# Optimization experiments

Hardware: AMD Instinct MI355X
Metric: run time of the kernel (lower is better)

The kernel has to match this reference:

```python
import jax, jax.numpy as jnp
import numpy as np

B, C, H, W_IMG, P, D = 64, 3, 224, 224, 16, 768
N_PATCH = (H // P) * (W_IMG // P)  # 196
SEQ = N_PATCH + 1                  # 197


def setup_inputs() -> dict:
    key = jax.random.key(0)
    k1, k2, k3, k4, k5 = jax.random.split(key, 5)
    in_feat = P * P * C  # 768
    return {
        "x": jax.random.normal(k1, (B, C, H, W_IMG), dtype=jnp.float32),
        "W": jax.random.normal(k2, (in_feat, D), dtype=jnp.float32) * (1.0 / np.sqrt(in_feat)),
        "b": jax.random.normal(k3, (D,), dtype=jnp.float32) * 0.02,
        "pos_table": jax.random.normal(k4, (SEQ, D), dtype=jnp.float32) * 0.02,
        "class_token": jax.random.normal(k5, (1, 1, D), dtype=jnp.float32),
    }


def _patchify(x):
    # Matches torch loop: patch (i,j) is x[:, :, i*P:(i+1)*P, j*P:(j+1)*P].reshape(B, C*P*P)
    # i.e. features ordered channel-major then row then col within patch.
    b = x.shape[0]
    hp, wp = H // P, W_IMG // P
    x = x.reshape(b, C, hp, P, wp, P)              # (B,C,hp,P,wp,P)
    x = x.transpose(0, 2, 4, 1, 3, 5)              # (B,hp,wp,C,P,P)
    return x.reshape(b, hp * wp, C * P * P)        # (B,N,C*P*P)


def reference(x, W, b, pos_table, class_token):
    patches = _patchify(x)                          # (B, N, C*P*P)
    tokens = jnp.einsum("bnf,fd->bnd", patches, W) + b  # (B, N, D)
    cls = jnp.broadcast_to(class_token, (x.shape[0], 1, D))
    seq = jnp.concatenate([cls, tokens], axis=1)    # (B, SEQ, D)
    # positions = arange(SEQ) broadcast over batch -> embedding lookup
    return seq + pos_table[None, :, :]              # dropout is identity in eval
```

## Files before the change

kernel.cpp:

```cpp
#include <hip/hip_runtime.h>
#include <hip/hip_bf16.h>

namespace {

constexpr int Bsz = 64, Cch = 3, Himg = 224, Wimg = 224, Ppat = 16;
constexpr int Dm = 768, NPW = 14, NPATCH = 196, SEQn = 197;
constexpr int Mtot = Bsz * NPATCH;
constexpr int Ktot = 768, Ntot = 768;
constexpr int BM = 64, BN = 128, BK = 64;
constexpr int MT = Mtot / BM;
constexpr int NT = Ntot / BN;
constexpr int KT = Ktot / BK;
constexpr int NBLK = MT * NT;
constexpr int TA = BM * BK;
constexpr int TB = BN * BK;
constexpr size_t AP_ELEMS = (size_t)MT * KT * TA;
constexpr size_t WT_ELEMS = (size_t)NT * KT * TB;
constexpr size_t WS_NEED = (AP_ELEMS + WT_ELEMS) * 2;
constexpr int WPREP_BLK = (Ktot / 8) * Ntot / 256;
constexpr int CLS_BLK = Bsz * Dm / 256;

typedef __attribute__((ext_vector_type(8))) short bf16x8;
typedef __attribute__((ext_vector_type(4))) float f32x4;

__device__ inline unsigned short f2bf(float f) {
  __bf16 h = (__bf16)f;
  union { __bf16 h; unsigned short u; } c;
  c.h = h;
  return c.u;
}

__global__ void prep_kernel(const float* __restrict__ x, const float* __restrict__ W,
                            const float* __restrict__ pos, const float* __restrict__ cls,
                            unsigned short* __restrict__ Ap, unsigned short* __restrict__ Wt,
                            float* __restrict__ out, int nPatchBlk) {
  __shared__ unsigned short tile[TA];
  const int bid = blockIdx.x;
  const int t = threadIdx.x;
  if (bid < nPatchBlk) {
    int mt = bid / KT, kt = bid - mt * KT;
    int ml = t >> 2, ks = t & 3;
    int m = mt * BM + ml;
    int b = m / NPATCH;
    int pidx = m - b * NPATCH;
    int ph = pidx / NPW, pw = pidx - ph * NPW;
    int kbase = kt * BK + ks * 16;
    int c = kbase >> 8, pi = (kbase >> 4) & 15;
    const float* src = x + (((size_t)(b * Cch + c) * Himg + ph * Ppat + pi) * Wimg + pw * Ppat);
#pragma unroll
    for (int j = 0; j < 4; ++j) {
      float4 v = *reinterpret_cast<const float4*>(src + 4 * j);
      int idx = (ml * BK + ks * 16 + 4 * j) ^ ((ml & 7) << 3);
      *reinterpret_cast<ushort4*>(&tile[idx]) =
          make_ushort4(f2bf(v.x), f2bf(v.y), f2bf(v.z), f2bf(v.w));
    }
    __syncthreads();
    const uint4* sp = reinterpret_cast<const uint4*>(tile);
    uint4* dp = reinterpret_cast<uint4*>(Ap + (size_t)bid * TA);
    dp[t] = sp[t];
    dp[t + 256] = sp[t + 256];
  } else if (bid < nPatchBlk + WPREP_BLK) {
    int cid = (bid - nPatchBlk) * 256 + t;
    int kc = cid / Ntot;
    int n = cid - kc * Ntot;
    int nb = n >> 7;
    int np = n & 127;
    int kt = kc >> 3;
    int k8 = (kc & 7) * 8;
    unsigned short tmp[8];
#pragma unroll
    for (int j = 0; j < 8; ++j) tmp[j] = f2bf(W[(kc * 8 + j) * Ntot + n]);
    int idx = np * BK + k8;
    int sidx = idx ^ ((np & 7) << 3);
    unsigned short* dst = Wt + (size_t)(nb * KT + kt) * TB + sidx;
    *reinterpret_cast<ushort4*>(dst + 0) = make_ushort4(tmp[0], tmp[1], tmp[2], tmp[3]);
    *reinterpret_cast<ushort4*>(dst + 4) = make_ushort4(tmp[4], tmp[5], tmp[6], tmp[7]);
  } else {
    int i = (bid - nPatchBlk - WPREP_BLK) * 256 + t;
    int b = i / Dm;
    int d = i - b * Dm;
    out[(size_t)b * (SEQn * Dm) + d] = cls[d] + pos[d];
  }
}

__global__ __launch_bounds__(256, 3)
void gemm_kernel(const unsigned short* __restrict__ Ap, const unsigned short* __restrict__ Wt,
                 const float* __restrict__ bias, const float* __restrict__ pos,
                 float* __restrict__ out) {
  __shared__ unsigned short A[2][TA];
  __shared__ unsigned short B[2][TB];

  const int orig = blockIdx.x;
  const int wg = (orig & 7) * (NBLK / 8) + (orig >> 3);
  const int bm = wg / NT;
  const int bn = wg - bm * NT;

  const int t = threadIdx.x;
  const int lane = t & 63;
  const int wid = t >> 6;
  const int wr = wid >> 1, wc = wid & 1;
  const int fr = lane & 15, fq = lane >> 4;

  const unsigned short* aSrc = Ap + (size_t)(bm * KT) * TA + t * 8;
  const unsigned short* bSrc = Wt + (size_t)(bn * KT) * TB + t * 8;

  auto STAGEA = [&](int buf, int kt) {
#pragma unroll
    for (int i = 0; i < 2; ++i)
      __builtin_amdgcn_global_load_lds(
          (const __attribute__((address_space(1))) unsigned int*)(aSrc + kt * TA + i * 2048),
          (__attribute__((address_space(3))) unsigned int*)(&A[buf][t * 8 + i * 2048]),
          16, 0, 0);
  };
  auto STAGEB = [&](int buf, int kt) {
#pragma unroll
    for (int i = 0; i < 4; ++i)
      __builtin_amdgcn_global_load_lds(
          (const __attribute__((address_space(1))) unsigned int*)(bSrc + kt * TB + i * 2048),
          (__attribute__((address_space(3))) unsigned int*)(&B[buf][t * 8 + i * 2048]),
          16, 0, 0);
  };

  f32x4 acc[2][4];
#pragma unroll
  for (int mi = 0; mi < 2; ++mi)
#pragma unroll
    for (int ni = 0; ni < 4; ++ni) acc[mi][ni] = {0.f, 0.f, 0.f, 0.f};

  STAGEA(0, 0);
  STAGEB(0, 0);
  __syncthreads();

  for (int kt = 0; kt < KT; ++kt) {
    const int cur = kt & 1, nxt = cur ^ 1;
    if (kt + 1 < KT) {
      STAGEA(nxt, kt + 1);
      STAGEB(nxt, kt + 1);
    }
#pragma unroll
    for (int ks = 0; ks < 2; ++ks) {
      bf16x8 af[2], bfr[4];
#pragma unroll
      for (int mi = 0; mi < 2; ++mi) {
        int row = wr * 32 + mi * 16 + fr;
        int idx = (row * BK + ks * 32 + fq * 8) ^ ((row & 7) << 3);
        af[mi] = *reinterpret_cast<const bf16x8*>(&A[cur][idx]);
      }
#pragma unroll
      for (int ni = 0; ni < 4; ++ni) {
        int n = wc * 64 + ni * 16 + fr;
        int idx = (n * BK + ks * 32 + fq * 8) ^ ((n & 7) << 3);
        bfr[ni] = *reinterpret_cast<const bf16x8*>(&B[cur][idx]);
      }
#pragma unroll
      for (int mi = 0; mi < 2; ++mi)
#pragma unroll
        for (int ni = 0; ni < 4; ++ni)
          acc[mi][ni] = __builtin_amdgcn_mfma_f32_16x16x32_bf16(
              af[mi], bfr[ni], acc[mi][ni], 0, 0, 0);
    }
    __syncthreads();
  }

  const int n0 = bn * BN + wc * 64;
  float bv[4];
#pragma unroll
  for (int ni = 0; ni < 4; ++ni) bv[ni] = bias[n0 + ni * 16 + fr];
#pragma unroll
  for (int mi = 0; mi < 2; ++mi) {
#pragma unroll
    for (int j = 0; j < 4; ++j) {
      int m = bm * BM + wr * 32 + mi * 16 + fq * 4 + j;
      int b = m / NPATCH;
      int s = m - b * NPATCH + 1;
      float* orow = out + ((size_t)b * SEQn + s) * Dm + n0;
      const float* prow = pos + (size_t)s * Dm + n0;
#pragma unroll
      for (int ni = 0; ni < 4; ++ni) {
        int d = ni * 16 + fr;
        orow[d] = acc[mi][ni][j] + bv[ni] + prow[d];
      }
    }
  }
}

__global__ __launch_bounds__(512, 6)
void gemm_fb(const float* __restrict__ x, const unsigned short* __restrict__ Wt,
             const float* __restrict__ bias, const float* __restrict__ pos,
             float* __restrict__ out) {
  __shared__ unsigned short As[2][TA];
  __shared__ unsigned short Bs[2][TB];

  const int orig = blockIdx.x;
  const int wg = (orig & 7) * (NBLK / 8) + (orig >> 3);
  const int bm = wg / NT;
  const int bn = wg - bm * NT;

  const int t = threadIdx.x;
  const int lane = t & 63;
  const int wid = t >> 6;
  const int wr = wid >> 2, wc = wid & 3;
  const int fr = lane & 15, fq = lane >> 4;

  const int c4 = t & 15;
  const int r0 = t >> 4;
  int a_base[2];
#pragma unroll
  for (int i = 0; i < 2; ++i) {
    int m = bm * BM + r0 + 32 * i;
    int b = m / NPATCH;
    int pidx = m - b * NPATCH;
    int ph = pidx / NPW;
    int pw = pidx - ph * NPW;
    a_base[i] = ((b * Cch) * Himg + ph * Ppat) * Wimg + pw * Ppat;
  }
  const unsigned short* wt_base = Wt + (size_t)bn * (KT * TB);

  float4 av[2];
  auto LOADA = [&](int kt) {
    int kg = kt * BK + c4 * 4;
    int c = kg >> 8;
    int pi = (kg >> 4) & 15;
    int pj = kg & 15;
    int off = (c * Himg + pi) * Wimg + pj;
#pragma unroll
    for (int i = 0; i < 2; ++i)
      av[i] = *reinterpret_cast<const float4*>(x + a_base[i] + off);
  };
  auto WRITEA = [&](int buf) {
#pragma unroll
    for (int i = 0; i < 2; ++i) {
      int row = r0 + 32 * i;
      int idx = (row * BK + c4 * 4) ^ ((row & 7) << 3);
      ushort4 pk = make_ushort4(f2bf(av[i].x), f2bf(av[i].y), f2bf(av[i].z), f2bf(av[i].w));
      *reinterpret_cast<ushort4*>(&As[buf][idx]) = pk;
    }
  };
  auto STAGEB = [&](int buf, int kt) {
    const unsigned short* src = wt_base + kt * TB + t * 8;
#pragma unroll
    for (int i = 0; i < 2; ++i) {
      __builtin_amdgcn_global_load_lds(
          (const __attribute__((address_space(1))) unsigned int*)(src + i * 4096),
          (__attribute__((address_space(3))) unsigned int*)(&Bs[buf][t * 8 + i * 4096]),
          16, 0, 0);
    }
  };

  f32x4 acc[2][2];
#pragma unroll
  for (int mi = 0; mi < 2; ++mi)
#pragma unroll
    for (int ni = 0; ni < 2; ++ni) acc[mi][ni] = {0.f, 0.f, 0.f, 0.f};

  LOADA(0);
  STAGEB(0, 0);
  WRITEA(0);
  __syncthreads();

  for (int kt = 0; kt < KT; ++kt) {
    const int cur = kt & 1, nxt = cur ^ 1;
    if (kt + 1 < KT) {
      LOADA(kt + 1);
      STAGEB(nxt, kt + 1);
    }
#pragma unroll
    for (int ks = 0; ks < 2; ++ks) {
      bf16x8 af[2], bfr[2];
#pragma unroll
      for (int mi = 0; mi < 2; ++mi) {
        int row = wr * 32 + mi * 16 + fr;
        int idx = (row * BK + ks * 32 + fq * 8) ^ ((row & 7) << 3);
        af[mi] = *reinterpret_cast<const bf16x8*>(&As[cur][idx]);
      }
#pragma unroll
      for (int ni = 0; ni < 2; ++ni) {
        int n = wc * 32 + ni * 16 + fr;
        int idx = (n * BK + ks * 32 + fq * 8) ^ ((n & 7) << 3);
        bfr[ni] = *reinterpret_cast<const bf16x8*>(&Bs[cur][idx]);
      }
#pragma unroll
      for (int mi = 0; mi < 2; ++mi)
#pragma unroll
        for (int ni = 0; ni < 2; ++ni)
          acc[mi][ni] = __builtin_amdgcn_mfma_f32_16x16x32_bf16(
              af[mi], bfr[ni], acc[mi][ni], 0, 0, 0);
    }
    if (kt + 1 < KT) WRITEA(nxt);
    __syncthreads();
  }

  const int n0 = bn * BN + wc * 32;
  float bv[2];
#pragma unroll
  for (int ni = 0; ni < 2; ++ni) bv[ni] = bias[n0 + ni * 16 + fr];
#pragma unroll
  for (int mi = 0; mi < 2; ++mi) {
#pragma unroll
    for (int j = 0; j < 4; ++j) {
      int m = bm * BM + wr * 32 + mi * 16 + fq * 4 + j;
      int b = m / NPATCH;
      int s = m - b * NPATCH + 1;
      float* orow = out + ((size_t)b * SEQn + s) * Dm + n0;
      const float* prow = pos + (size_t)s * Dm + n0;
#pragma unroll
      for (int ni = 0; ni < 2; ++ni) {
        int d = ni * 16 + fr;
        orow[d] = acc[mi][ni][j] + bv[ni] + prow[d];
      }
    }
  }
}

}

extern "C" void kernel_launch(void* const* d_in, const int* in_sizes, int n_in,
                              void* d_out, int out_size, void* d_ws, size_t ws_size,
                              hipStream_t stream) {
  const float* x = (const float*)d_in[0];
  const float* W = (const float*)d_in[1];
  const float* bias = (const float*)d_in[2];
  const float* pos = (const float*)d_in[3];
  const float* cls = (const float*)d_in[4];
  float* out = (float*)d_out;

  const bool pure = ws_size >= WS_NEED;
  unsigned short* Ap = (unsigned short*)d_ws;
  unsigned short* Wt = pure ? Ap + AP_ELEMS : Ap;
  const int nPatchBlk = pure ? MT * KT : 0;

  prep_kernel<<<nPatchBlk + WPREP_BLK + CLS_BLK, 256, 0, stream>>>(
      x, W, pos, cls, Ap, Wt, out, nPatchBlk);
  if (pure)
    gemm_kernel<<<NBLK, 256, 0, stream>>>(Ap, Wt, bias, pos, out);
  else
    gemm_fb<<<NBLK, 512, 0, stream>>>(x, Wt, bias, pos, out);
}
```

Baseline: 44.79 us.

## Enlarge GEMM M-tile to 128 and write patch tiles directly without LDS

Doubles the GEMM block tile in M from 64 to 128, so each wave computes a 64x64 sub-tile with 16 accumulators, cutting the number of blocks and the B-tile reloads per output. The prep kernel now swizzles patch data straight to global memory in 16-byte stores instead of staging through shared memory, and the W prep uses one 16-byte store. The XCD block remap is generalised for a block count not divisible by 8, and the fallback kernel keeps its own 64-row constants. Fewer blocks (588 versus 1176) and more registers per thread under launch_bounds(256,2) may lower occupancy and leave CUs unevenly loaded.

```diff
diff --git a/kernel.cpp b/kernel.cpp
--- a/kernel.cpp
+++ b/kernel.cpp
@@ -7,16 +7,17 @@
 constexpr int Dm = 768, NPW = 14, NPATCH = 196, SEQn = 197;
 constexpr int Mtot = Bsz * NPATCH;
 constexpr int Ktot = 768, Ntot = 768;
-constexpr int BM = 64, BN = 128, BK = 64;
+constexpr int BM = 128, BN = 128, BK = 64;
 constexpr int MT = Mtot / BM;
 constexpr int NT = Ntot / BN;
 constexpr int KT = Ktot / BK;
 constexpr int NBLK = MT * NT;
-constexpr int TA = BM * BK;
+constexpr int TAm = BM * BK;
 constexpr int TB = BN * BK;
-constexpr size_t AP_ELEMS = (size_t)MT * KT * TA;
+constexpr size_t AP_ELEMS = (size_t)MT * KT * TAm;
 constexpr size_t WT_ELEMS = (size_t)NT * KT * TB;
 constexpr size_t WS_NEED = (AP_ELEMS + WT_ELEMS) * 2;
+constexpr int PATCH_BLK = MT * KT;
 constexpr int WPREP_BLK = (Ktot / 8) * Ntot / 256;
 constexpr int CLS_BLK = Bsz * Dm / 256;
 
@@ -30,35 +31,43 @@
   return c.u;
 }
 
+union Pack8 { unsigned short s[8]; uint4 v; };
+
 __global__ void prep_kernel(const float* __restrict__ x, const float* __restrict__ W,
                             const float* __restrict__ pos, const float* __restrict__ cls,
                             unsigned short* __restrict__ Ap, unsigned short* __restrict__ Wt,
                             float* __restrict__ out, int nPatchBlk) {
-  __shared__ unsigned short tile[TA];
   const int bid = blockIdx.x;
   const int t = threadIdx.x;
   if (bid < nPatchBlk) {
     int mt = bid / KT, kt = bid - mt * KT;
-    int ml = t >> 2, ks = t & 3;
-    int m = mt * BM + ml;
-    int b = m / NPATCH;
-    int pidx = m - b * NPATCH;
-    int ph = pidx / NPW, pw = pidx - ph * NPW;
-    int kbase = kt * BK + ks * 16;
-    int c = kbase >> 8, pi = (kbase >> 4) & 15;
-    const float* src = x + (((size_t)(b * Cch + c) * Himg + ph * Ppat + pi) * Wimg + pw * Ppat);
-#pragma unroll
-    for (int j = 0; j < 4; ++j) {
-      float4 v = *reinterpret_cast<const float4*>(src + 4 * j);
-      int idx = (ml * BK + ks * 16 + 4 * j) ^ ((ml & 7) << 3);
-      *reinterpret_cast<ushort4*>(&tile[idx]) =
-          make_ushort4(f2bf(v.x), f2bf(v.y), f2bf(v.z), f2bf(v.w));
-    }
-    __syncthreads();
-    const uint4* sp = reinterpret_cast<const uint4*>(tile);
-    uint4* dp = reinterpret_cast<uint4*>(Ap + (size_t)bid * TA);
-    dp[t] = sp[t];
-    dp[t + 256] = sp[t + 256];
+    int r_ = t >> 2, ks = t & 3;
+#pragma unroll
+    for (int it = 0; it < 2; ++it) {
+      int r = r_ + 64 * it;
+      int m = mt * BM + r;
+      int b = m / NPATCH;
+      int pidx = m - b * NPATCH;
+      int ph = pidx / NPW, pw = pidx - ph * NPW;
+      int kg = kt * BK + ks * 16;
+      int c = kg >> 8, pi = (kg >> 4) & 15;
+      const float* src = x + ((size_t)(b * Cch + c) * Himg + ph * Ppat + pi) * Wimg
+                         + pw * Ppat;
+      float4 v0 = *reinterpret_cast<const float4*>(src + 0);
+      float4 v1 = *reinterpret_cast<const float4*>(src + 4);
+      float4 v2 = *reinterpret_cast<const float4*>(src + 8);
+      float4 v3 = *reinterpret_cast<const float4*>(src + 12);
+      Pack8 p0, p1;
+      p0.s[0] = f2bf(v0.x); p0.s[1] = f2bf(v0.y); p0.s[2] = f2bf(v0.z); p0.s[3] = f2bf(v0.w);
+      p0.s[4] = f2bf(v1.x); p0.s[5] = f2bf(v1.y); p0.s[6] = f2bf(v1.z); p0.s[7] = f2bf(v1.w);
+      p1.s[0] = f2bf(v2.x); p1.s[1] = f2bf(v2.y); p1.s[2] = f2bf(v2.z); p1.s[3] = f2bf(v2.w);
+      p1.s[4] = f2bf(v3.x); p1.s[5] = f2bf(v3.y); p1.s[6] = f2bf(v3.z); p1.s[7] = f2bf(v3.w);
+      unsigned short* dst = Ap + (size_t)bid * TAm;
+      int g = r * BK + ks * 16;
+      int sw = (r & 7) << 3;
+      *reinterpret_cast<uint4*>(dst + (g ^ sw)) = p0.v;
+      *reinterpret_cast<uint4*>(dst + ((g + 8) ^ sw)) = p1.v;
+    }
   } else if (bid < nPatchBlk + WPREP_BLK) {
     int cid = (bid - nPatchBlk) * 256 + t;
     int kc = cid / Ntot;
@@ -67,14 +76,11 @@
     int np = n & 127;
     int kt = kc >> 3;
     int k8 = (kc & 7) * 8;
-    unsigned short tmp[8];
-#pragma unroll
-    for (int j = 0; j < 8; ++j) tmp[j] = f2bf(W[(kc * 8 + j) * Ntot + n]);
-    int idx = np * BK + k8;
-    int sidx = idx ^ ((np & 7) << 3);
-    unsigned short* dst = Wt + (size_t)(nb * KT + kt) * TB + sidx;
-    *reinterpret_cast<ushort4*>(dst + 0) = make_ushort4(tmp[0], tmp[1], tmp[2], tmp[3]);
-    *reinterpret_cast<ushort4*>(dst + 4) = make_ushort4(tmp[4], tmp[5], tmp[6], tmp[7]);
+    Pack8 p;
+#pragma unroll
+    for (int j = 0; j < 8; ++j) p.s[j] = f2bf(W[(size_t)(kc * 8 + j) * Ntot + n]);
+    int sidx = (np * BK + k8) ^ ((np & 7) << 3);
+    *reinterpret_cast<uint4*>(Wt + (size_t)(nb * KT + kt) * TB + sidx) = p.v;
   } else {
     int i = (bid - nPatchBlk - WPREP_BLK) * 256 + t;
     int b = i / Dm;
@@ -83,15 +89,17 @@
   }
 }
 
-__global__ __launch_bounds__(256, 3)
+__global__ __launch_bounds__(256, 2)
 void gemm_kernel(const unsigned short* __restrict__ Ap, const unsigned short* __restrict__ Wt,
                  const float* __restrict__ bias, const float* __restrict__ pos,
                  float* __restrict__ out) {
-  __shared__ unsigned short A[2][TA];
+  __shared__ unsigned short A[2][TAm];
   __shared__ unsigned short B[2][TB];
 
   const int orig = blockIdx.x;
-  const int wg = (orig & 7) * (NBLK / 8) + (orig >> 3);
+  const int xcd = orig & 7;
+  constexpr int Q = NBLK >> 3, R = NBLK & 7;
+  const int wg = (xcd < R ? xcd * (Q + 1) : R * (Q + 1) + (xcd - R) * Q) + (orig >> 3);
   const int bm = wg / NT;
   const int bn = wg - bm * NT;
 
@@ -101,18 +109,16 @@
   const int wr = wid >> 1, wc = wid & 1;
   const int fr = lane & 15, fq = lane >> 4;
 
-  const unsigned short* aSrc = Ap + (size_t)(bm * KT) * TA + t * 8;
+  const unsigned short* aSrc = Ap + (size_t)(bm * KT) * TAm + t * 8;
   const unsigned short* bSrc = Wt + (size_t)(bn * KT) * TB + t * 8;
 
-  auto STAGEA = [&](int buf, int kt) {
-#pragma unroll
-    for (int i = 0; i < 2; ++i)
+  auto STAGE = [&](int buf, int kt) {
+#pragma unroll
+    for (int i = 0; i < 4; ++i)
       __builtin_amdgcn_global_load_lds(
-          (const __attribute__((address_space(1))) unsigned int*)(aSrc + kt * TA + i * 2048),
+          (const __attribute__((address_space(1))) unsigned int*)(aSrc + kt * TAm + i * 2048),
           (__attribute__((address_space(3))) unsigned int*)(&A[buf][t * 8 + i * 2048]),
           16, 0, 0);
-  };
-  auto STAGEB = [&](int buf, int kt) {
 #pragma unroll
     for (int i = 0; i < 4; ++i)
       __builtin_amdgcn_global_load_lds(
@@ -121,28 +127,24 @@
           16, 0, 0);
   };
 
-  f32x4 acc[2][4];
-#pragma unroll
-  for (int mi = 0; mi < 2; ++mi)
+  f32x4 acc[4][4];
+#pragma unroll
+  for (int mi = 0; mi < 4; ++mi)
 #pragma unroll
     for (int ni = 0; ni < 4; ++ni) acc[mi][ni] = {0.f, 0.f, 0.f, 0.f};
 
-  STAGEA(0, 0);
-  STAGEB(0, 0);
+  STAGE(0, 0);
   __syncthreads();
 
   for (int kt = 0; kt < KT; ++kt) {
     const int cur = kt & 1, nxt = cur ^ 1;
-    if (kt + 1 < KT) {
-      STAGEA(nxt, kt + 1);
-      STAGEB(nxt, kt + 1);
-    }
+    if (kt + 1 < KT) STAGE(nxt, kt + 1);
 #pragma unroll
     for (int ks = 0; ks < 2; ++ks) {
-      bf16x8 af[2], bfr[4];
-#pragma unroll
-      for (int mi = 0; mi < 2; ++mi) {
-        int row = wr * 32 + mi * 16 + fr;
+      bf16x8 af[4], bfr[4];
+#pragma unroll
+      for (int mi = 0; mi < 4; ++mi) {
+        int row = wr * 64 + mi * 16 + fr;
         int idx = (row * BK + ks * 32 + fq * 8) ^ ((row & 7) << 3);
         af[mi] = *reinterpret_cast<const bf16x8*>(&A[cur][idx]);
       }
@@ -153,7 +155,7 @@
         bfr[ni] = *reinterpret_cast<const bf16x8*>(&B[cur][idx]);
       }
 #pragma unroll
-      for (int mi = 0; mi < 2; ++mi)
+      for (int mi = 0; mi < 4; ++mi)
 #pragma unroll
         for (int ni = 0; ni < 4; ++ni)
           acc[mi][ni] = __builtin_amdgcn_mfma_f32_16x16x32_bf16(
@@ -167,10 +169,10 @@
 #pragma unroll
   for (int ni = 0; ni < 4; ++ni) bv[ni] = bias[n0 + ni * 16 + fr];
 #pragma unroll
-  for (int mi = 0; mi < 2; ++mi) {
+  for (int mi = 0; mi < 4; ++mi) {
 #pragma unroll
     for (int j = 0; j < 4; ++j) {
-      int m = bm * BM + wr * 32 + mi * 16 + fq * 4 + j;
+      int m = bm * BM + wr * 64 + mi * 16 + fq * 4 + j;
       int b = m / NPATCH;
       int s = m - b * NPATCH + 1;
       float* orow = out + ((size_t)b * SEQn + s) * Dm + n0;
@@ -188,13 +190,15 @@
 void gemm_fb(const float* __restrict__ x, const unsigned short* __restrict__ Wt,
              const float* __restrict__ bias, const float* __restrict__ pos,
              float* __restrict__ out) {
-  __shared__ unsigned short As[2][TA];
+  constexpr int FBM = 64, FNT = 6, FNBLK = (Mtot / FBM) * FNT;
+  constexpr int FTA = FBM * BK;
+  __shared__ unsigned short As[2][FTA];
   __shared__ unsigned short Bs[2][TB];
 
   const int orig = blockIdx.x;
-  const int wg = (orig & 7) * (NBLK / 8) + (orig >> 3);
-  const int bm = wg / NT;
-  const int bn = wg - bm * NT;
+  const int wg = (orig & 7) * (FNBLK / 8) + (orig >> 3);
+  const int bm = wg / FNT;
+  const int bn = wg - bm * FNT;
 
   const int t = threadIdx.x;
   const int lane = t & 63;
@@ -207,7 +211,7 @@
   int a_base[2];
 #pragma unroll
   for (int i = 0; i < 2; ++i) {
-    int m = bm * BM + r0 + 32 * i;
+    int m = bm * FBM + r0 + 32 * i;
     int b = m / NPATCH;
     int pidx = m - b * NPATCH;
     int ph = pidx / NPW;
@@ -219,9 +223,7 @@
   float4 av[2];
   auto LOADA = [&](int kt) {
     int kg = kt * BK + c4 * 4;
-    int c = kg >> 8;
-    int pi = (kg >> 4) & 15;
-    int pj = kg & 15;
+    int c = kg >> 8, pi = (kg >> 4) & 15, pj = kg & 15;
     int off = (c * Himg + pi) * Wimg + pj;
 #pragma unroll
     for (int i = 0; i < 2; ++i)
@@ -298,7 +300,7 @@
   for (int mi = 0; mi < 2; ++mi) {
 #pragma unroll
     for (int j = 0; j < 4; ++j) {
-      int m = bm * BM + wr * 32 + mi * 16 + fq * 4 + j;
+      int m = bm * FBM + wr * 32 + mi * 16 + fq * 4 + j;
       int b = m / NPATCH;
       int s = m - b * NPATCH + 1;
       float* orow = out + ((size_t)b * SEQn + s) * Dm + n0;
@@ -327,12 +329,12 @@
   const bool pure = ws_size >= WS_NEED;
   unsigned short* Ap = (unsigned short*)d_ws;
   unsigned short* Wt = pure ? Ap + AP_ELEMS : Ap;
-  const int nPatchBlk = pure ? MT * KT : 0;
+  const int nPatchBlk = pure ? PATCH_BLK : 0;
 
   prep_kernel<<<nPatchBlk + WPREP_BLK + CLS_BLK, 256, 0, stream>>>(
       x, W, pos, cls, Ap, Wt, out, nPatchBlk);
   if (pure)
     gemm_kernel<<<NBLK, 256, 0, stream>>>(Ap, Wt, bias, pos, out);
   else
-    gemm_fb<<<NBLK, 512, 0, stream>>>(x, Wt, bias, pos, out);
-}
+    gemm_fb<<<1176, 512, 0, stream>>>(x, Wt, bias, pos, out);
+}
```

Result: slower. 52.55 us (+17.3%).
